# Kernel optimization log

Measured on AMD Instinct MI355X. Metric: run time of the kernel, lower is better.

## Reference

```python
import jax, jax.numpy as jnp
import numpy as np

B, T, E, H, OUT = 64, 2048, 512, 32, 131


def setup_inputs() -> dict:
    key = jax.random.key(0)
    ks = jax.random.split(key, 12)
    x = jax.random.normal(ks[0], (B, T, E), dtype=jnp.float32)
    # pack_padded_sequence(enforce_sorted=True) requires descending lengths
    src_len = jnp.sort(jax.random.randint(ks[1], (B,), 1, T + 1))[::-1]
    other_input = jax.random.normal(ks[2], (B, OUT), dtype=jnp.float32)
    s_ih, s_hh = 1.0 / np.sqrt(E), 1.0 / np.sqrt(H)
    W_ih_f = jax.random.normal(ks[3], (3 * H, E), dtype=jnp.float32) * s_ih
    W_hh_f = jax.random.normal(ks[4], (3 * H, H), dtype=jnp.float32) * s_hh
    b_ih_f = jax.random.normal(ks[5], (3 * H,), dtype=jnp.float32) * s_hh
    b_hh_f = jax.random.normal(ks[6], (3 * H,), dtype=jnp.float32) * s_hh
    W_ih_b = jax.random.normal(ks[7], (3 * H, E), dtype=jnp.float32) * s_ih
    W_hh_b = jax.random.normal(ks[8], (3 * H, H), dtype=jnp.float32) * s_hh
    b_ih_b = jax.random.normal(ks[9], (3 * H,), dtype=jnp.float32) * s_hh
    b_hh_b = jax.random.normal(ks[10], (3 * H,), dtype=jnp.float32) * s_hh
    fc_W = jax.random.normal(ks[11], (OUT, 2 * H), dtype=jnp.float32) * (1.0 / np.sqrt(2 * H))
    fc_b = jnp.zeros((OUT,), dtype=jnp.float32)
    return {"x": x, "src_len": src_len, "other_input": other_input,
            "W_ih_f": W_ih_f, "W_hh_f": W_hh_f, "b_ih_f": b_ih_f, "b_hh_f": b_hh_f,
            "W_ih_b": W_ih_b, "W_hh_b": W_hh_b, "b_ih_b": b_ih_b, "b_hh_b": b_hh_b,
            "fc_W": fc_W, "fc_b": fc_b}


def _gru_dir(x_proj, W_hh, b_hh, lengths, reverse):
    # x_proj: [B,T,3H] precomputed input gates; mask updates where t < length
    xs = jnp.swapaxes(x_proj, 0, 1)  # [T,B,3H]
    ts = jnp.arange(xs.shape[0])
    if reverse:
        xs, ts = xs[::-1], ts[::-1]

    def step(h, inp):
        gx, t = inp
        gh = h @ W_hh.T + b_hh
        xr, xz, xn = jnp.split(gx, 3, axis=-1)
        hr, hz, hn = jnp.split(gh, 3, axis=-1)
        r = jax.nn.sigmoid(xr + hr)
        z = jax.nn.sigmoid(xz + hz)
        n = jnp.tanh(xn + r * hn)
        h_new = (1.0 - z) * n + z * h
        mask = (t < lengths)[:, None]
        return jnp.where(mask, h_new, h), None

    h0 = jnp.zeros((x_proj.shape[0], W_hh.shape[1]), dtype=x_proj.dtype)
    h, _ = jax.lax.scan(step, h0, (xs, ts))
    return h  # [B,H] final hidden of this direction


def reference(x, src_len, other_input, W_ih_f, W_hh_f, b_ih_f, b_hh_f,
              W_ih_b, W_hh_b, b_ih_b, b_hh_b, fc_W, fc_b):
    lengths = src_len.astype(jnp.int32)
    # batched input projections (the only big GEMMs)
    xp_f = jnp.einsum('bte,ge->btg', x, W_ih_f) + b_ih_f  # [B,T,3H]
    xp_b = jnp.einsum('bte,ge->btg', x, W_ih_b) + b_ih_b
    h_f = _gru_dir(xp_f, W_hh_f, b_hh_f, lengths, reverse=False)
    h_b = _gru_dir(xp_b, W_hh_b, b_hh_b, lengths, reverse=True)
    # hidden_state[-2]=fwd, hidden_state[-1]=bwd for 1-layer bidirectional GRU
    hidden = jnp.concatenate([h_f, h_b], axis=1)  # [B,2H]
    return hidden @ fc_W.T + fc_b  # [B,OUT]
```

## Files before the change

kernel.cpp:

```cpp
#include <hip/hip_runtime.h>
#include <hip/hip_bf16.h>
#include <cstddef>
#include <cstdint>

typedef __bf16 bf16_t;
typedef __attribute__((ext_vector_type(8))) __bf16 bf16x8;
typedef __attribute__((ext_vector_type(4))) float f32x4;
typedef __attribute__((ext_vector_type(2))) unsigned u32x2;

#define B_  64
#define T_  2048
#define E_  512
#define H_  32
#define G_  96
#define N2_ 192
#define OUT_ 131

#define C1_ (-1.44269504088896340736f)
#define C2_ ( 2.88539008177792681472f)

__global__ void prep_kernel(const float* __restrict__ Wf, const float* __restrict__ Wb,
                            const float* __restrict__ bf_, const float* __restrict__ bb_,
                            bf16_t* __restrict__ Wbf, float* __restrict__ bias) {
    int idx = blockIdx.x * 256 + threadIdx.x;
    int g = idx >> 9, k = idx & 511;
    float v = (g < G_) ? Wf[g * E_ + k] : Wb[(g - G_) * E_ + k];
    Wbf[idx] = (bf16_t)v;
    if (idx < N2_) bias[idx] = (idx < G_) ? bf_[idx] : bb_[idx - G_];
}

__global__ __launch_bounds__(256) void proj_kernel(
    const float* __restrict__ x,
    const bf16_t* __restrict__ Wbf,
    const float* __restrict__ bias,
    float* __restrict__ xp)
{
    __shared__ bf16_t Alds[64][72];
    __shared__ bf16_t Blds[96][72];

    const int tid  = threadIdx.x;
    const int lane = tid & 63;
    const int w    = tid >> 6;
    const int wm   = w & 1;
    const int wn   = w >> 1;
    const int m0   = blockIdx.x * 64;
    const int n0   = blockIdx.y * 96;

    const int arow = tid >> 2;
    const int acol = (tid & 3) * 16;

    f32x4 acc[2][3];
    #pragma unroll
    for (int i = 0; i < 2; ++i)
        #pragma unroll
        for (int jn = 0; jn < 3; ++jn)
            acc[i][jn] = (f32x4){0.f, 0.f, 0.f, 0.f};

    for (int kt = 0; kt < 8; ++kt) {
        const int c0 = kt * 64;
        __syncthreads();
        {
            const float* asrc = x + (size_t)(m0 + arow) * E_ + c0 + acol;
            float4 v0 = *(const float4*)(asrc + 0);
            float4 v1 = *(const float4*)(asrc + 4);
            float4 v2 = *(const float4*)(asrc + 8);
            float4 v3 = *(const float4*)(asrc + 12);
            bf16x8 pa, pb;
            pa[0]=(bf16_t)v0.x; pa[1]=(bf16_t)v0.y; pa[2]=(bf16_t)v0.z; pa[3]=(bf16_t)v0.w;
            pa[4]=(bf16_t)v1.x; pa[5]=(bf16_t)v1.y; pa[6]=(bf16_t)v1.z; pa[7]=(bf16_t)v1.w;
            pb[0]=(bf16_t)v2.x; pb[1]=(bf16_t)v2.y; pb[2]=(bf16_t)v2.z; pb[3]=(bf16_t)v2.w;
            pb[4]=(bf16_t)v3.x; pb[5]=(bf16_t)v3.y; pb[6]=(bf16_t)v3.z; pb[7]=(bf16_t)v3.w;
            *(bf16x8*)&Alds[arow][acol]     = pa;
            *(bf16x8*)&Alds[arow][acol + 8] = pb;
        }
        #pragma unroll
        for (int i = 0; i < 3; ++i) {
            int u = tid + i * 256;
            int brow = u >> 3, koff = (u & 7) * 8;
            bf16x8 bv = *(const bf16x8*)(Wbf + (size_t)(n0 + brow) * E_ + c0 + koff);
            *(bf16x8*)&Blds[brow][koff] = bv;
        }
        __syncthreads();
        #pragma unroll
        for (int ks = 0; ks < 2; ++ks) {
            bf16x8 af[2], bfr[3];
            #pragma unroll
            for (int i = 0; i < 2; ++i)
                af[i] = *(const bf16x8*)&Alds[wm * 32 + i * 16 + (lane & 15)][ks * 32 + (lane >> 4) * 8];
            #pragma unroll
            for (int jn = 0; jn < 3; ++jn)
                bfr[jn] = *(const bf16x8*)&Blds[wn * 48 + jn * 16 + (lane & 15)][ks * 32 + (lane >> 4) * 8];
            #pragma unroll
            for (int i = 0; i < 2; ++i)
                #pragma unroll
                for (int jn = 0; jn < 3; ++jn)
                    acc[i][jn] = __builtin_amdgcn_mfma_f32_16x16x32_bf16(af[i], bfr[jn], acc[i][jn], 0, 0, 0);
        }
    }
    #pragma unroll
    for (int i = 0; i < 2; ++i)
        #pragma unroll
        for (int jn = 0; jn < 3; ++jn)
            #pragma unroll
            for (int r = 0; r < 4; ++r) {
                int mg = m0 + wm * 32 + i * 16 + (lane >> 4) * 4 + r;
                int ng = n0 + wn * 48 + jn * 16 + (lane & 15);
                int lg = (ng >= 96) ? ng - 96 : ng;
                float scl = (lg < 64) ? C1_ : C2_;
                xp[(size_t)mg * N2_ + ng] = scl * (acc[i][jn][r] + bias[ng]);
            }
}

__global__ __launch_bounds__(64) void gru_rec_kernel(
    const float* __restrict__ xp,
    const int*   __restrict__ src_len,
    const float* __restrict__ Whh_f, const float* __restrict__ bhh_f,
    const float* __restrict__ Whh_b, const float* __restrict__ bhh_b,
    float* __restrict__ hout)
{
    const int blk  = blockIdx.x;
    const int b    = blk >> 1;
    const int dir  = blk & 1;
    const int l    = threadIdx.x;
    const int l15  = l & 15;
    const int p    = (l >> 4) & 1;
    const int j    = l15 + 16 * (l >> 5);

    const float* Whh = dir ? Whh_b : Whh_f;
    const float* bhh = dir ? bhh_b : bhh_f;

    int s_dir;
    {
        int q1 = __builtin_amdgcn_update_dpp(l15, l15, 0x121, 0xf, 0xf, false);
        s_dir = (__builtin_amdgcn_readfirstlane(q1) == 1) ? 1 : -1;
    }

    float wr[16], wz[16], wn[16];
    #pragma unroll
    for (int i = 0; i < 16; ++i) {
        int k = 16 * p + ((l15 + s_dir * i) & 15);
        wr[i] = C1_ * Whh[(j)      * H_ + k];
        wz[i] = C1_ * Whh[(32 + j) * H_ + k];
        wn[i] = C2_ * Whh[(64 + j) * H_ + k];
    }
    const float brh = 0.5f * C1_ * bhh[j];
    const float bzh = 0.5f * C1_ * bhh[32 + j];
    const float bnh = 0.5f * C2_ * bhh[64 + j];

#if __has_builtin(__builtin_amdgcn_permlane32_swap)
    bool m0c, m1c;
    {
        unsigned xg = (unsigned)(l >> 5);
        u32x2 pr = __builtin_amdgcn_permlane32_swap(xg, xg, false, false);
        unsigned ag = pr.x;
        unsigned d  = (unsigned)p;
        m0c = (xg == d);
        m1c = (ag == d);
    }
#endif

    int len = src_len[b];
    if (len < 1) len = 1;
    if (len > T_) len = T_;
    len = __builtin_amdgcn_readfirstlane(len);
    const int sd = dir ? -1 : 1;
    const int t0 = dir ? (len - 1) : 0;
    const float* colp = xp + (size_t)b * (T_ * N2_) + dir * G_ + j;

    float hval = 0.0f;
    float vrot = 0.0f;

    auto loadq = [&](int q, float& xr, float& xz, float& xn) {
        int qq = (q < len) ? q : (len - 1);
        int t  = t0 + sd * qq;
        const float* ps = colp + (size_t)t * N2_;
        xr = ps[0]; xz = ps[32]; xn = ps[64];
    };

    auto pl16sum = [&](float a) -> float {
#if __has_builtin(__builtin_amdgcn_permlane16_swap)
        u32x2 rr = __builtin_amdgcn_permlane16_swap(__float_as_uint(a), __float_as_uint(a), false, false);
        return __uint_as_float(rr.x) + __uint_as_float(rr.y);
#else
        return a + __int_as_float(__builtin_amdgcn_ds_bpermute((l ^ 16) << 2, __float_as_int(a)));
#endif
    };

    auto step = [&](float xr, float xz, float xn) {
        float cur = vrot;
        float ar = brh, az = bzh, an = bnh;
        #pragma unroll
        for (int i = 0; i < 16; ++i) {
            if (i) cur = __int_as_float(__builtin_amdgcn_update_dpp(
                        __float_as_int(cur), __float_as_int(cur), 0x121, 0xf, 0xf, false));
            ar = __builtin_fmaf(cur, wr[i], ar);
            az = __builtin_fmaf(cur, wz[i], az);
            an = __builtin_fmaf(cur, wn[i], an);
        }
        float arf = pl16sum(ar) + xr;
        float azf = pl16sum(az) + xz;
        float anf = pl16sum(an);
        float er = __builtin_amdgcn_exp2f(arf);
        float r  = __builtin_amdgcn_rcpf(1.0f + er);
        float ez = __builtin_amdgcn_exp2f(azf);
        float z  = __builtin_amdgcn_rcpf(1.0f + ez);
        float na = __builtin_fmaf(r, anf, xn);
        float eu = __builtin_amdgcn_exp2f(na);
        float u  = __builtin_amdgcn_rcpf(1.0f + eu);
        float hpe = hval + ez;
        float t2  = __builtin_fmaf(-2.0f * ez, u, hpe);
        hval = z * t2;
#if __has_builtin(__builtin_amdgcn_permlane32_swap)
        u32x2 sw = __builtin_amdgcn_permlane32_swap(__float_as_uint(hval), __float_as_uint(hval), false, false);
        float av = __uint_as_float(sw.x);
        float bv = __uint_as_float(sw.y);
        float ts = m1c ? av : bv;
        vrot = m0c ? hval : ts;
#else
        vrot = __int_as_float(__builtin_amdgcn_ds_bpermute((l15 + 32 * p) << 2, __float_as_int(hval)));
#endif
    };

    float bxr[4], bxz[4], bxn[4];
    #pragma unroll
    for (int d = 0; d < 4; ++d) loadq(d, bxr[d], bxz[d], bxn[d]);
    int s = 0;
    while (s + 4 <= len) {
        #pragma unroll
        for (int d = 0; d < 4; ++d) {
            step(bxr[d], bxz[d], bxn[d]);
            loadq(s + d + 4, bxr[d], bxz[d], bxn[d]);
        }
        s += 4;
    }
    #pragma unroll
    for (int d = 0; d < 4; ++d)
        if (s + d < len) step(bxr[d], bxz[d], bxn[d]);

    if (p == 0) hout[b * 64 + dir * 32 + j] = hval;
}

__global__ __launch_bounds__(192) void fc_kernel(
    const float* __restrict__ hbuf,
    const float* __restrict__ fcW,
    const float* __restrict__ fcb,
    float* __restrict__ out)
{
    __shared__ float hrow[64];
    const int b = blockIdx.x, tid = threadIdx.x;
    if (tid < 64) hrow[tid] = hbuf[b * 64 + tid];
    __syncthreads();
    if (tid < OUT_) {
        float acc = fcb[tid];
        #pragma unroll
        for (int i = 0; i < 64; ++i)
            acc = __builtin_fmaf(hrow[i], fcW[tid * 64 + i], acc);
        out[b * OUT_ + tid] = acc;
    }
}

extern "C" void kernel_launch(void* const* d_in, const int* in_sizes, int n_in,
                              void* d_out, int out_size, void* d_ws, size_t ws_size,
                              hipStream_t stream) {
    const float* x    = (const float*)d_in[0];
    const int*   srcl = (const int*)  d_in[1];
    const float* Wihf = (const float*)d_in[3];
    const float* Whhf = (const float*)d_in[4];
    const float* bihf = (const float*)d_in[5];
    const float* bhhf = (const float*)d_in[6];
    const float* Wihb = (const float*)d_in[7];
    const float* Whhb = (const float*)d_in[8];
    const float* bihb = (const float*)d_in[9];
    const float* bhhb = (const float*)d_in[10];
    const float* fcW  = (const float*)d_in[11];
    const float* fcb  = (const float*)d_in[12];
    float* out = (float*)d_out;

    const size_t XP_BYTES   = (size_t)B_ * T_ * N2_ * 4;
    const size_t HBUF_BYTES = (size_t)B_ * 64 * 4;
    const size_t BIAS_BYTES = 1024;
    const size_t WBF_BYTES  = (size_t)N2_ * E_ * 2;
    if (ws_size < XP_BYTES + HBUF_BYTES + BIAS_BYTES + WBF_BYTES) return;

    char* ws = (char*)d_ws;
    float*  xp   = (float*)ws;
    float*  hbuf = (float*)(ws + XP_BYTES);
    float*  bias = (float*)(ws + XP_BYTES + HBUF_BYTES);
    bf16_t* Wbf  = (bf16_t*)(ws + XP_BYTES + HBUF_BYTES + BIAS_BYTES);

    prep_kernel<<<384, 256, 0, stream>>>(Wihf, Wihb, bihf, bihb, Wbf, bias);
    dim3 pg((B_ * T_) / 64, 2);
    proj_kernel<<<pg, 256, 0, stream>>>(x, Wbf, bias, xp);
    gru_rec_kernel<<<B_ * 2, 64, 0, stream>>>(xp, srcl, Whhf, bhhf, Whhb, bhhb, hbuf);
    fc_kernel<<<B_, 192, 0, stream>>>(hbuf, fcW, fcb, out);
}
```

Before: 566.7 us.

## Run both GRU directions in one wave with packed FMA matvec

The recurrence kernel now gives each batch row one 64-lane wave: the lower 32 lanes run the forward direction and the upper 32 the backward one, each lane owning one hidden unit. Every lane computes its full 32-wide dot product as two packed f32x2 FMA halves, using a permlane16 swap to fetch the other half of h and inline-asm DPP row rotations. This drops the cross-lane partial-sum reductions and the permlane32 redistribution from each serial step, and halves the number of blocks. The trade is more weight registers per lane and one kernel with a latency-bound chain per batch row instead of two.

```diff
diff --git a/kernel.cpp b/kernel.cpp
--- a/kernel.cpp
+++ b/kernel.cpp
@@ -6,6 +6,7 @@
 typedef __bf16 bf16_t;
 typedef __attribute__((ext_vector_type(8))) __bf16 bf16x8;
 typedef __attribute__((ext_vector_type(4))) float f32x4;
+typedef __attribute__((ext_vector_type(2))) float f32x2;
 typedef __attribute__((ext_vector_type(2))) unsigned u32x2;
 
 #define B_  64
@@ -18,6 +19,10 @@
 
 #define C1_ (-1.44269504088896340736f)
 #define C2_ ( 2.88539008177792681472f)
+
+#define MOVDPP(out_, in_, N_)                                               \
+    asm("v_mov_b32_dpp %0, %1 row_ror:" #N_ " row_mask:0xf bank_mask:0xf"   \
+        : "=v"(out_) : "v"(in_))
 
 __global__ void prep_kernel(const float* __restrict__ Wf, const float* __restrict__ Wb,
                             const float* __restrict__ bf_, const float* __restrict__ bb_,
@@ -118,44 +123,42 @@
     const float* __restrict__ Whh_b, const float* __restrict__ bhh_b,
     float* __restrict__ hout)
 {
-    const int blk  = blockIdx.x;
-    const int b    = blk >> 1;
-    const int dir  = blk & 1;
+    const int b    = blockIdx.x;
     const int l    = threadIdx.x;
     const int l15  = l & 15;
-    const int p    = (l >> 4) & 1;
-    const int j    = l15 + 16 * (l >> 5);
-
-    const float* Whh = dir ? Whh_b : Whh_f;
-    const float* bhh = dir ? bhh_b : bhh_f;
+    const int half = l >> 5;
+    const int rr   = (l >> 4) & 1;
+    const int j    = l & 31;
+
+    const float* Whh = half ? Whh_b : Whh_f;
+    const float* bhh = half ? bhh_b : bhh_f;
 
     int s_dir;
     {
-        int q1 = __builtin_amdgcn_update_dpp(l15, l15, 0x121, 0xf, 0xf, false);
+        int q1;
+        MOVDPP(q1, l15, 1);
         s_dir = (__builtin_amdgcn_readfirstlane(q1) == 1) ? 1 : -1;
     }
 
-    float wr[16], wz[16], wn[16];
+    f32x2 wrp[16], wzp[16], wnp[16];
     #pragma unroll
     for (int i = 0; i < 16; ++i) {
-        int k = 16 * p + ((l15 + s_dir * i) & 15);
-        wr[i] = C1_ * Whh[(j)      * H_ + k];
-        wz[i] = C1_ * Whh[(32 + j) * H_ + k];
-        wn[i] = C2_ * Whh[(64 + j) * H_ + k];
-    }
-    const float brh = 0.5f * C1_ * bhh[j];
-    const float bzh = 0.5f * C1_ * bhh[32 + j];
-    const float bnh = 0.5f * C2_ * bhh[64 + j];
-
-#if __has_builtin(__builtin_amdgcn_permlane32_swap)
-    bool m0c, m1c;
+        int c  = (l15 + s_dir * i) & 15;
+        int ka = rr * 16 + c;
+        int kb = (1 - rr) * 16 + c;
+        wrp[i] = (f32x2){C1_ * Whh[(j)      * H_ + ka], C1_ * Whh[(j)      * H_ + kb]};
+        wzp[i] = (f32x2){C1_ * Whh[(32 + j) * H_ + ka], C1_ * Whh[(32 + j) * H_ + kb]};
+        wnp[i] = (f32x2){C2_ * Whh[(64 + j) * H_ + ka], C2_ * Whh[(64 + j) * H_ + kb]};
+    }
+    const float br = C1_ * bhh[j];
+    const float bz = C1_ * bhh[32 + j];
+    const float bn = C2_ * bhh[64 + j];
+
+#if __has_builtin(__builtin_amdgcn_permlane16_swap)
+    bool useX;
     {
-        unsigned xg = (unsigned)(l >> 5);
-        u32x2 pr = __builtin_amdgcn_permlane32_swap(xg, xg, false, false);
-        unsigned ag = pr.x;
-        unsigned d  = (unsigned)p;
-        m0c = (xg == d);
-        m1c = (ag == d);
+        u32x2 pr = __builtin_amdgcn_permlane16_swap((unsigned)l, (unsigned)l, false, false);
+        useX = (pr.x == (unsigned)(l ^ 16));
     }
 #endif
 
@@ -163,62 +166,64 @@
     if (len < 1) len = 1;
     if (len > T_) len = T_;
     len = __builtin_amdgcn_readfirstlane(len);
-    const int sd = dir ? -1 : 1;
-    const int t0 = dir ? (len - 1) : 0;
-    const float* colp = xp + (size_t)b * (T_ * N2_) + dir * G_ + j;
+
+    const float* pb = xp + (size_t)b * (T_ * N2_) + half * G_ + j;
 
     float hval = 0.0f;
-    float vrot = 0.0f;
 
     auto loadq = [&](int q, float& xr, float& xz, float& xn) {
         int qq = (q < len) ? q : (len - 1);
-        int t  = t0 + sd * qq;
-        const float* ps = colp + (size_t)t * N2_;
+        int t  = half ? (len - 1 - qq) : qq;
+        const float* ps = pb + (size_t)t * N2_;
         xr = ps[0]; xz = ps[32]; xn = ps[64];
     };
 
-    auto pl16sum = [&](float a) -> float {
+    auto step = [&](float xr, float xz, float xn) {
+        float hB;
 #if __has_builtin(__builtin_amdgcn_permlane16_swap)
-        u32x2 rr = __builtin_amdgcn_permlane16_swap(__float_as_uint(a), __float_as_uint(a), false, false);
-        return __uint_as_float(rr.x) + __uint_as_float(rr.y);
+        {
+            u32x2 sw = __builtin_amdgcn_permlane16_swap(
+                __float_as_uint(hval), __float_as_uint(hval), false, false);
+            hB = __uint_as_float(useX ? sw.x : sw.y);
+        }
 #else
-        return a + __int_as_float(__builtin_amdgcn_ds_bpermute((l ^ 16) << 2, __float_as_int(a)));
+        hB = __int_as_float(__builtin_amdgcn_ds_bpermute((l ^ 16) << 2, __float_as_int(hval)));
 #endif
-    };
-
-    auto step = [&](float xr, float xz, float xn) {
-        float cur = vrot;
-        float ar = brh, az = bzh, an = bnh;
-        #pragma unroll
-        for (int i = 0; i < 16; ++i) {
-            if (i) cur = __int_as_float(__builtin_amdgcn_update_dpp(
-                        __float_as_int(cur), __float_as_int(cur), 0x121, 0xf, 0xf, false));
-            ar = __builtin_fmaf(cur, wr[i], ar);
-            az = __builtin_fmaf(cur, wz[i], az);
-            an = __builtin_fmaf(cur, wn[i], an);
-        }
-        float arf = pl16sum(ar) + xr;
-        float azf = pl16sum(az) + xz;
-        float anf = pl16sum(an);
-        float er = __builtin_amdgcn_exp2f(arf);
-        float r  = __builtin_amdgcn_rcpf(1.0f + er);
-        float ez = __builtin_amdgcn_exp2f(azf);
-        float z  = __builtin_amdgcn_rcpf(1.0f + ez);
-        float na = __builtin_fmaf(r, anf, xn);
+        f32x2 acr = (f32x2){br, 0.f};
+        f32x2 acz = (f32x2){bz, 0.f};
+        f32x2 acn = (f32x2){bn, 0.f};
+        {
+            f32x2 hp = (f32x2){hval, hB};
+            acr = __builtin_elementwise_fma(hp, wrp[0], acr);
+            acz = __builtin_elementwise_fma(hp, wzp[0], acz);
+            acn = __builtin_elementwise_fma(hp, wnp[0], acn);
+        }
+#define STEPI(N_)                                                   \
+        {   float ra_, rb_;                                         \
+            MOVDPP(ra_, hval, N_);                                  \
+            MOVDPP(rb_, hB,   N_);                                  \
+            f32x2 hp_ = (f32x2){ra_, rb_};                          \
+            acr = __builtin_elementwise_fma(hp_, wrp[N_], acr);     \
+            acz = __builtin_elementwise_fma(hp_, wzp[N_], acz);     \
+            acn = __builtin_elementwise_fma(hp_, wnp[N_], acn);     \
+        }
+        STEPI(1)  STEPI(2)  STEPI(3)  STEPI(4)  STEPI(5)
+        STEPI(6)  STEPI(7)  STEPI(8)  STEPI(9)  STEPI(10)
+        STEPI(11) STEPI(12) STEPI(13) STEPI(14) STEPI(15)
+#undef STEPI
+        float ar = acr.x + acr.y + xr;
+        float az = acz.x + acz.y + xz;
+        float an = acn.x + acn.y;
+        float er = __builtin_amdgcn_exp2f(ar);
+        float rg = __builtin_amdgcn_rcpf(1.0f + er);
+        float ez = __builtin_amdgcn_exp2f(az);
+        float zg = __builtin_amdgcn_rcpf(1.0f + ez);
+        float na = __builtin_fmaf(rg, an, xn);
         float eu = __builtin_amdgcn_exp2f(na);
         float u  = __builtin_amdgcn_rcpf(1.0f + eu);
-        float hpe = hval + ez;
-        float t2  = __builtin_fmaf(-2.0f * ez, u, hpe);
-        hval = z * t2;
-#if __has_builtin(__builtin_amdgcn_permlane32_swap)
-        u32x2 sw = __builtin_amdgcn_permlane32_swap(__float_as_uint(hval), __float_as_uint(hval), false, false);
-        float av = __uint_as_float(sw.x);
-        float bv = __uint_as_float(sw.y);
-        float ts = m1c ? av : bv;
-        vrot = m0c ? hval : ts;
-#else
-        vrot = __int_as_float(__builtin_amdgcn_ds_bpermute((l15 + 32 * p) << 2, __float_as_int(hval)));
-#endif
+        float m2 = -(ez + ez);
+        float hp = hval + ez;
+        hval = zg * __builtin_fmaf(m2, u, hp);
     };
 
     float bxr[4], bxz[4], bxn[4];
@@ -237,7 +242,7 @@
     for (int d = 0; d < 4; ++d)
         if (s + d < len) step(bxr[d], bxz[d], bxn[d]);
 
-    if (p == 0) hout[b * 64 + dir * 32 + j] = hval;
+    hout[b * 64 + half * 32 + j] = hval;
 }
 
 __global__ __launch_bounds__(192) void fc_kernel(
@@ -291,6 +296,6 @@
     prep_kernel<<<384, 256, 0, stream>>>(Wihf, Wihb, bihf, bihb, Wbf, bias);
     dim3 pg((B_ * T_) / 64, 2);
     proj_kernel<<<pg, 256, 0, stream>>>(x, Wbf, bias, xp);
-    gru_rec_kernel<<<B_ * 2, 64, 0, stream>>>(xp, srcl, Whhf, bhhf, Whhb, bhhb, hbuf);
+    gru_rec_kernel<<<B_, 64, 0, stream>>>(xp, srcl, Whhf, bhhf, Whhb, bhhb, hbuf);
     fc_kernel<<<B_, 192, 0, stream>>>(hbuf, fcW, fcb, out);
 }
```

Result: slower. 580.5 us (+2.4%).
